# Performance work log

Hardware: AMD Instinct MI355X
Metric: run time of the kernel (lower is better)

## Reference

```python
import jax, jax.numpy as jnp
import numpy as np
from jax import lax

N, C, H, W = 4, 256, 64, 64
R = 2          # upsample ratio (scale_factor)
K = 5          # CARAFE up_kernel
COMP = 64      # CARAFEPack compressed_channels
EPS = 1e-5     # BatchNorm eps


def setup_inputs() -> dict:
    key = jax.random.key(0)
    ks = jax.random.split(key, 8)
    w = lambda k, s: jax.random.normal(k, s, jnp.float32) * 0.05
    return {
        "low_feature": jax.random.normal(ks[0], (N, C, H * R, W * R), jnp.float32),
        "high_feature": jax.random.normal(ks[1], (N, C, H, W), jnp.float32),
        "w_cc": w(ks[2], (COMP, C, 1, 1)),            # channel compressor 1x1
        "b_cc": jnp.zeros((COMP,), jnp.float32),
        "w_ce": w(ks[3], (K * K * R * R, COMP, 3, 3)), # content encoder 3x3
        "b_ce": jnp.zeros((K * K * R * R,), jnp.float32),
        "w_conv2": w(ks[4], (C, C, 1, 1)),
        "b_conv2": jnp.zeros((C,), jnp.float32),
        "w_bott": w(ks[5], (C, 2 * C, 1, 1)),          # bottleneck 1x1, no bias
        "gamma": jnp.ones((C,), jnp.float32),
        "beta": jnp.zeros((C,), jnp.float32),
    }


def _conv1x1(x, w, b=None):
    y = jnp.einsum('nchw,oc->nohw', x, w[:, :, 0, 0])
    if b is not None:
        y = y + b[None, :, None, None]
    return y


def _conv3x3(x, w, b):
    y = lax.conv_general_dilated(x, w, (1, 1), [(1, 1), (1, 1)],
                                 dimension_numbers=('NCHW', 'OIHW', 'NCHW'))
    return y + b[None, :, None, None]


def _pixel_shuffle(x, r):
    n, c, h, w = x.shape
    c2 = c // (r * r)
    x = x.reshape(n, c2, r, r, h, w).transpose(0, 1, 4, 2, 5, 3)
    return x.reshape(n, c2, h * r, w * r)


def _carafe(x, w_cc, b_cc, w_ce, b_ce):
    n, c, h, w = x.shape
    # predicted kernels: compress -> encode -> pixel_shuffle -> softmax over k^2
    mask = _conv3x3(_conv1x1(x, w_cc, b_cc), w_ce, b_ce)      # [N, K*K*R*R, H, W]
    mask = _pixel_shuffle(mask, R)                            # [N, K*K, H*R, W*R]
    mask = jax.nn.softmax(mask, axis=1)                       # group=1 -> over K*K
    # k x k neighborhoods of x (zero-padded), kernel index = ky*K + kx
    pad = K // 2
    xp = jnp.pad(x, ((0, 0), (0, 0), (pad, pad), (pad, pad)))
    patches = jnp.stack([xp[:, :, dy:dy + h, dx:dx + w]
                         for dy in range(K) for dx in range(K)], axis=2)  # [N,C,K*K,H,W]
    # each output pixel (i,j) reads source (i//R, j//R) neighborhood
    mr = mask.reshape(n, K * K, h, R, w, R)
    out = jnp.einsum('nckhw,nkhawb->nchawb', patches, mr)
    return out.reshape(n, c, h * R, w * R)


def reference(low_feature, high_feature, w_cc, b_cc, w_ce, b_ce,
              w_conv2, b_conv2, w_bott, gamma, beta):
    hf = _carafe(high_feature, w_cc, b_cc, w_ce, b_ce)        # [N,C,H*R,W*R]
    value = _conv1x1(hf, w_conv2, b_conv2)
    x = jnp.concatenate([value, hf], axis=1)                  # [N,2C,.,.]
    x = _conv1x1(x, w_bott)
    # BatchNorm (training-mode batch statistics) + ReLU
    mean = jnp.mean(x, axis=(0, 2, 3), keepdims=True)
    var = jnp.var(x, axis=(0, 2, 3), keepdims=True)
    x = (x - mean) * lax.rsqrt(var + EPS)
    x = x * gamma[None, :, None, None] + beta[None, :, None, None]
    return jax.nn.relu(x)
```

## Files before the change

### kernel.cpp

```cpp
#include <hip/hip_runtime.h>
#include <hip/hip_bf16.h>

#define N_    4
#define C_    256
#define PS_   4096
#define PO_   16384
#define COMP_ 64
#define QCH_  100

typedef unsigned short u16;
typedef __attribute__((ext_vector_type(8))) short short8;
typedef __attribute__((ext_vector_type(4))) float f32x4;

__device__ __forceinline__ u16 f2bu(float f) {
    __hip_bfloat16 h = __float2bfloat16(f);
    return __builtin_bit_cast(u16, h);
}
__device__ __forceinline__ float bits2f(unsigned u) {
    union { unsigned i; float f; } v; v.i = u; return v.f;
}

__global__ __launch_bounds__(256) void k_prep(const float* __restrict__ w_bott,
        const float* __restrict__ w_conv2, const float* __restrict__ b_conv2,
        const float* __restrict__ w_ce, const float* __restrict__ w_cc,
        u16* __restrict__ Weff_bf, float* __restrict__ beff,
        u16* __restrict__ Wb, u16* __restrict__ Wcc_bf) {
    int bid = blockIdx.x;
    if (bid < 256) {
        int o = bid, c = threadIdx.x;
        __shared__ float wb[512];
        wb[c]       = w_bott[o * 512 + c];
        wb[c + 256] = w_bott[o * 512 + 256 + c];
        __syncthreads();
        float acc = wb[256 + c];
        #pragma unroll 8
        for (int m = 0; m < 256; ++m)
            acc += wb[m] * w_conv2[m * 256 + c];
        Weff_bf[o * 256 + c] = f2bu(acc);
        if (c == 0) {
            float be = 0.f;
            for (int m = 0; m < 256; ++m) be += wb[m] * b_conv2[m];
            beff[o] = be;
        }
    } else if (bid < 544) {
        int i = (bid - 256) * 256 + threadIdx.x;
        int q = i / 576, u = i - q * 576;
        float v = (q < 100) ? w_ce[q * 576 + u] : 0.f;
        Wb[i] = f2bu(v);
    } else {
        int j = (bid - 544) * 256 + threadIdx.x;
        Wcc_bf[j] = f2bu(w_cc[j]);
    }
}

__global__ __launch_bounds__(256) void k_compress_mfma(const u16* __restrict__ Wcc_bf,
        const float* __restrict__ high, const float* __restrict__ b_cc,
        float* __restrict__ comp) {
    int tid = threadIdx.x;
    int wid = tid >> 6, lane = tid & 63;
    int col = lane & 15, quad = lane >> 4;
    int px0 = blockIdx.x * 64;
    int n = px0 >> 12, pxb = px0 & 4095;
    __shared__ u16 As[64 * 40];
    __shared__ u16 Bs[64 * 40];
    f32x4 acc[4] = {};
    #pragma unroll 1
    for (int k0 = 0; k0 < 256; k0 += 32) {
        __syncthreads();
        {
            int row = tid >> 2, seg = tid & 3;
            short8 av = *reinterpret_cast<const short8*>(Wcc_bf + row * 256 + k0 + seg * 8);
            *reinterpret_cast<short8*>(&As[row * 40 + seg * 8]) = av;
        }
        #pragma unroll
        for (int it = 0; it < 4; ++it) {
            int idx = it * 256 + tid;
            int c = (idx >> 6) * 2, px = idx & 63;
            const float* hp = high + (n * C_ + k0 + c) * PS_ + pxb + px;
            unsigned lo = f2bu(hp[0]);
            unsigned hi = f2bu(hp[PS_]);
            *reinterpret_cast<unsigned*>(&Bs[px * 40 + c]) = lo | (hi << 16);
        }
        __syncthreads();
        short8 a = *reinterpret_cast<const short8*>(&As[(wid * 16 + col) * 40 + quad * 8]);
        #pragma unroll
        for (int nt = 0; nt < 4; ++nt) {
            short8 b = *reinterpret_cast<const short8*>(&Bs[(nt * 16 + col) * 40 + quad * 8]);
            acc[nt] = __builtin_amdgcn_mfma_f32_16x16x32_bf16(a, b, acc[nt], 0, 0, 0);
        }
    }
    #pragma unroll
    for (int r = 0; r < 4; ++r) {
        int m = wid * 16 + quad * 4 + r;
        float bias = b_cc[m];
        float* cp = comp + (n * COMP_ + m) * PS_ + pxb + col;
        #pragma unroll
        for (int nt = 0; nt < 4; ++nt)
            cp[nt * 16] = acc[nt][r] + bias;
    }
}

__global__ __launch_bounds__(256) void k_im2col(const float* __restrict__ comp,
        u16* __restrict__ Icol) {
    int b = blockIdx.x;
    int n = b >> 6, tile = b & 63;
    int ty0 = (tile >> 3) << 3, tx0 = (tile & 7) << 3;
    int tid = threadIdx.x;
    __shared__ float ct[64 * 100];
    for (int idx = tid; idx < 6400; idx += 256) {
        int cc = idx / 100, r = idx - cc * 100;
        int yy = ty0 - 1 + r / 10, xx = tx0 - 1 + (r % 10);
        float v = 0.f;
        if ((unsigned)yy < 64u && (unsigned)xx < 64u)
            v = comp[(n * COMP_ + cc) * PS_ + yy * 64 + xx];
        ct[idx] = v;
    }
    __syncthreads();
    int u0 = tid * 2, u1 = u0 + 1;
    int c0 = (unsigned)u0 / 9u, t0 = u0 - c0 * 9;
    int c1 = (unsigned)u1 / 9u, t1 = u1 - c1 * 9;
    int off0 = c0 * 100 + (t0 / 3) * 10 + (t0 % 3);
    int off1 = c1 * 100 + (t1 / 3) * 10 + (t1 % 3);
    int u2 = 512 + tid * 2, u3 = u2 + 1;
    int c2 = (unsigned)u2 / 9u, t2 = u2 - c2 * 9;
    int c3 = (unsigned)u3 / 9u, t3 = u3 - c3 * 9;
    int off2 = c2 * 100 + (t2 / 3) * 10 + (t2 % 3);
    int off3 = c3 * 100 + (t3 / 3) * 10 + (t3 % 3);
    #pragma unroll 1
    for (int px = 0; px < 64; ++px) {
        int py = px >> 3, pxx = px & 7;
        int base = py * 10 + pxx;
        int gpx = n * PS_ + (ty0 + py) * 64 + tx0 + pxx;
        u16* dst = Icol + gpx * 576;
        unsigned lo = f2bu(ct[off0 + base]);
        unsigned hi = f2bu(ct[off1 + base]);
        *reinterpret_cast<unsigned*>(dst + u0) = lo | (hi << 16);
        if (tid < 32) {
            unsigned lo2 = f2bu(ct[off2 + base]);
            unsigned hi2 = f2bu(ct[off3 + base]);
            *reinterpret_cast<unsigned*>(dst + u2) = lo2 | (hi2 << 16);
        }
    }
}

__global__ __launch_bounds__(256) void k_encode_mfma(const u16* __restrict__ Wb,
        const u16* __restrict__ Icol, const float* __restrict__ b_ce,
        float* __restrict__ mask_raw) {
    int tid = threadIdx.x;
    int wid = tid >> 6, lane = tid & 63;
    int col = lane & 15, quad = lane >> 4;
    int px0 = blockIdx.x * 64;
    int n = px0 >> 12, pxb = px0 & 4095;
    __shared__ u16 As[128 * 40];
    __shared__ u16 Bs[64 * 40];
    f32x4 acc[2][4] = {};
    #pragma unroll 1
    for (int k0 = 0; k0 < 576; k0 += 32) {
        __syncthreads();
        #pragma unroll
        for (int it = 0; it < 2; ++it) {
            int s = tid + it * 256;
            int row = s >> 2, seg = s & 3;
            short8 av = *reinterpret_cast<const short8*>(Wb + row * 576 + k0 + seg * 8);
            *reinterpret_cast<short8*>(&As[row * 40 + seg * 8]) = av;
        }
        {
            int row = tid >> 2, seg = tid & 3;
            short8 bv = *reinterpret_cast<const short8*>(Icol + (px0 + row) * 576 + k0 + seg * 8);
            *reinterpret_cast<short8*>(&Bs[row * 40 + seg * 8]) = bv;
        }
        __syncthreads();
        short8 a0 = *reinterpret_cast<const short8*>(&As[(wid * 32 + col) * 40 + quad * 8]);
        short8 a1 = *reinterpret_cast<const short8*>(&As[(wid * 32 + 16 + col) * 40 + quad * 8]);
        #pragma unroll
        for (int nt = 0; nt < 4; ++nt) {
            short8 b = *reinterpret_cast<const short8*>(&Bs[(nt * 16 + col) * 40 + quad * 8]);
            acc[0][nt] = __builtin_amdgcn_mfma_f32_16x16x32_bf16(a0, b, acc[0][nt], 0, 0, 0);
            acc[1][nt] = __builtin_amdgcn_mfma_f32_16x16x32_bf16(a1, b, acc[1][nt], 0, 0, 0);
        }
    }
    #pragma unroll
    for (int mi = 0; mi < 2; ++mi) {
        int qbase = (wid * 2 + mi) * 16 + quad * 4;
        #pragma unroll
        for (int r = 0; r < 4; ++r) {
            int q = qbase + r;
            if (q < 100) {
                float bias = b_ce[q];
                float* mp = mask_raw + (n * QCH_ + q) * PS_ + pxb + col;
                #pragma unroll
                for (int nt = 0; nt < 4; ++nt)
                    mp[nt * 16] = acc[mi][nt][r] + bias;
            }
        }
    }
}

__global__ __launch_bounds__(256) void k_ygemm_mfma(const u16* __restrict__ Weff_bf,
        const float* __restrict__ high, u16* __restrict__ Yt) {
    int tid = threadIdx.x;
    int wid = tid >> 6, lane = tid & 63;
    int col = lane & 15, quad = lane >> 4;
    int px0 = blockIdx.x * 128;
    int o0 = blockIdx.y * 128;
    int n = px0 >> 12, pxb = px0 & 4095;
    __shared__ u16 As[128 * 40];
    __shared__ u16 Bs[128 * 40];
    f32x4 acc[2][8] = {};
    #pragma unroll 1
    for (int k0 = 0; k0 < 256; k0 += 32) {
        __syncthreads();
        #pragma unroll
        for (int it = 0; it < 2; ++it) {
            int s = tid + it * 256;
            int row = s >> 2, seg = s & 3;
            short8 av = *reinterpret_cast<const short8*>(Weff_bf + (o0 + row) * 256 + k0 + seg * 8);
            *reinterpret_cast<short8*>(&As[row * 40 + seg * 8]) = av;
        }
        #pragma unroll
        for (int it = 0; it < 8; ++it) {
            int idx = it * 256 + tid;
            int c = (idx >> 7) * 2, px = idx & 127;
            const float* hp = high + (n * C_ + k0 + c) * PS_ + pxb + px;
            unsigned lo = f2bu(hp[0]);
            unsigned hi = f2bu(hp[PS_]);
            *reinterpret_cast<unsigned*>(&Bs[px * 40 + c]) = lo | (hi << 16);
        }
        __syncthreads();
        short8 a0 = *reinterpret_cast<const short8*>(&As[(wid * 32 + col) * 40 + quad * 8]);
        short8 a1 = *reinterpret_cast<const short8*>(&As[(wid * 32 + 16 + col) * 40 + quad * 8]);
        #pragma unroll
        for (int nt = 0; nt < 8; ++nt) {
            short8 b = *reinterpret_cast<const short8*>(&Bs[(nt * 16 + col) * 40 + quad * 8]);
            acc[0][nt] = __builtin_amdgcn_mfma_f32_16x16x32_bf16(a0, b, acc[0][nt], 0, 0, 0);
            acc[1][nt] = __builtin_amdgcn_mfma_f32_16x16x32_bf16(a1, b, acc[1][nt], 0, 0, 0);
        }
    }
    #pragma unroll
    for (int mi = 0; mi < 2; ++mi) {
        int ob = o0 + wid * 32 + mi * 16 + quad * 4;
        #pragma unroll
        for (int nt = 0; nt < 8; ++nt) {
            int gpx = px0 + nt * 16 + col;
            unsigned lo = f2bu(acc[mi][nt][0]) | ((unsigned)f2bu(acc[mi][nt][1]) << 16);
            unsigned hi = f2bu(acc[mi][nt][2]) | ((unsigned)f2bu(acc[mi][nt][3]) << 16);
            uint2 pk; pk.x = lo; pk.y = hi;
            *reinterpret_cast<uint2*>(Yt + (size_t)gpx * 256 + ob) = pk;
        }
    }
}

__global__ __launch_bounds__(256, 4) void k_carafe(const u16* __restrict__ Yt,
        const float* __restrict__ mask_raw, const float* __restrict__ beff,
        float* __restrict__ xout, float* __restrict__ ps, float* __restrict__ pq) {
    int tile = blockIdx.x, n = blockIdx.y, zq = blockIdx.z;
    int sh0 = (tile >> 3) << 3, sw0 = (tile & 7) << 3;
    int tid = threadIdx.x;
    int px = tid & 63, g = tid >> 6;
    int ly = px >> 3, lx = px & 7;
    int h = sh0 + ly, w = sw0 + lx;
    int sp = (g & 1) << 1;
    int cg = (g >> 1) << 5;
    int ch0 = zq << 6;

    __shared__ u16 xt[144 * 68];

    const u16* Yb = Yt + (size_t)n * PS_ * 256;
    for (int idx = tid; idx < 1152; idx += 256) {
        int spix = idx >> 3, seg = idx & 7;
        int row = spix / 12, colm = spix - row * 12;
        int yy = sh0 - 2 + row, xx = sw0 - 2 + colm;
        short8 val = {};
        if ((unsigned)yy < 64u && (unsigned)xx < 64u)
            val = *reinterpret_cast<const short8*>(Yb + (size_t)(yy * 64 + xx) * 256 + ch0 + seg * 8);
        *reinterpret_cast<short8*>(&xt[spix * 68 + seg * 8]) = val;
    }

    float vs[2][25];
    {
        const float* mb = mask_raw + ((size_t)n * QCH_ + sp) * PS_ + h * 64 + w;
        #pragma unroll
        for (int j = 0; j < 2; ++j) {
            #pragma unroll
            for (int k = 0; k < 25; ++k)
                vs[j][k] = mb[(size_t)(k * 4 + j) * PS_];
            float mx = vs[j][0];
            #pragma unroll
            for (int k = 1; k < 25; ++k) mx = fmaxf(mx, vs[j][k]);
            float sum = 0.f;
            #pragma unroll
            for (int k = 0; k < 25; ++k) { vs[j][k] = __expf(vs[j][k] - mx); sum += vs[j][k]; }
            float inv = 1.f / sum;
            #pragma unroll
            for (int k = 0; k < 25; ++k) vs[j][k] *= inv;
        }
    }
    __syncthreads();

    const u16* bp = xt + (ly * 12 + lx) * 68;
    int row_off = (2 * h + (sp >> 1)) * 128 + 2 * w;
    int slot = (n * 64 + tile) * 2 + (g & 1);
    float* hp_base = xout + (size_t)n * C_ * PO_;

    #pragma unroll 1
    for (int cq = 0; cq < 8; ++cq) {
        int c = cg + cq * 4;
        int ch = ch0 + c;
        f32x4 bv = *reinterpret_cast<const f32x4*>(beff + ch);
        float a0[4] = {bv[0], bv[1], bv[2], bv[3]};
        float a1[4] = {bv[0], bv[1], bv[2], bv[3]};
        const u16* tp = bp + c;
        #pragma unroll
        for (int ky = 0; ky < 5; ++ky) {
            #pragma unroll
            for (int kx = 0; kx < 5; ++kx) {
                uint2 rv = *reinterpret_cast<const uint2*>(tp + (ky * 12 + kx) * 68);
                float f0 = bits2f(rv.x << 16);
                float f1 = bits2f(rv.x & 0xffff0000u);
                float f2 = bits2f(rv.y << 16);
                float f3 = bits2f(rv.y & 0xffff0000u);
                int k = ky * 5 + kx;
                float m0 = vs[0][k], m1 = vs[1][k];
                a0[0] += m0 * f0; a0[1] += m0 * f1;
                a0[2] += m0 * f2; a0[3] += m0 * f3;
                a1[0] += m1 * f0; a1[1] += m1 * f1;
                a1[2] += m1 * f2; a1[3] += m1 * f3;
            }
        }
        #pragma unroll
        for (int i = 0; i < 4; ++i) {
            float2 r; r.x = a0[i]; r.y = a1[i];
            *reinterpret_cast<float2*>(hp_base + (size_t)(ch + i) * PO_ + row_off) = r;
        }
        #pragma unroll
        for (int i = 0; i < 4; ++i) {
            float s  = a0[i] + a1[i];
            float q2 = a0[i] * a0[i] + a1[i] * a1[i];
            #pragma unroll
            for (int off = 1; off < 64; off <<= 1) {
                s  += __shfl_xor(s, off);
                q2 += __shfl_xor(q2, off);
            }
            if (px == 0) {
                ps[(ch + i) * 512 + slot] = s;
                pq[(ch + i) * 512 + slot] = q2;
            }
        }
    }
}

__global__ __launch_bounds__(256) void k_stats(const float* __restrict__ ps,
        const float* __restrict__ pq, const float* __restrict__ gamma,
        const float* __restrict__ beta, float* __restrict__ scale,
        float* __restrict__ shift) {
    int o = blockIdx.x, tid = threadIdx.x;
    float s = ps[o * 512 + tid] + ps[o * 512 + 256 + tid];
    float q = pq[o * 512 + tid] + pq[o * 512 + 256 + tid];
    __shared__ float rs[256], rq[256];
    rs[tid] = s; rq[tid] = q;
    __syncthreads();
    for (int off = 128; off > 0; off >>= 1) {
        if (tid < off) { rs[tid] += rs[tid + off]; rq[tid] += rq[tid + off]; }
        __syncthreads();
    }
    if (tid == 0) {
        float mean = rs[0] * (1.f / 65536.f);
        float var  = rq[0] * (1.f / 65536.f) - mean * mean;
        float sc = rsqrtf(var + 1e-5f) * gamma[o];
        scale[o] = sc;
        shift[o] = beta[o] - mean * sc;
    }
}

__global__ __launch_bounds__(256) void k_norm(float* __restrict__ xb,
        const float* __restrict__ scale, const float* __restrict__ shift) {
    int base = (blockIdx.x * 256 + threadIdx.x) * 4;
    int o = (base >> 14) & 255;
    float sc = scale[o], sh = shift[o];
    float4 v = *reinterpret_cast<const float4*>(xb + base);
    v.x = fmaxf(v.x * sc + sh, 0.f);
    v.y = fmaxf(v.y * sc + sh, 0.f);
    v.z = fmaxf(v.z * sc + sh, 0.f);
    v.w = fmaxf(v.w * sc + sh, 0.f);
    *reinterpret_cast<float4*>(xb + base) = v;
}

extern "C" void kernel_launch(void* const* d_in, const int* in_sizes, int n_in,
                              void* d_out, int out_size, void* d_ws, size_t ws_size,
                              hipStream_t stream) {
    const float* high    = (const float*)d_in[1];
    const float* w_cc    = (const float*)d_in[2];
    const float* b_cc    = (const float*)d_in[3];
    const float* w_ce    = (const float*)d_in[4];
    const float* b_ce    = (const float*)d_in[5];
    const float* w_conv2 = (const float*)d_in[6];
    const float* b_conv2 = (const float*)d_in[7];
    const float* w_bott  = (const float*)d_in[8];
    const float* gamma   = (const float*)d_in[9];
    const float* beta    = (const float*)d_in[10];

    char* ws = (char*)d_ws;
    float* beff    = (float*)(ws + 0);
    float* scale   = (float*)(ws + 1024);
    float* shift   = (float*)(ws + 2048);
    u16*   Weff_bf = (u16*)  (ws + 3072);
    u16*   Wcc_bf  = (u16*)  (ws + 134144);
    u16*   Wb      = (u16*)  (ws + 166912);
    float* mask    = (float*)(ws + 314368);
    float* comp    = (float*)(ws + 314368);
    u16*   Icol    = (u16*)  (ws + 6867968);
    u16*   Yt      = (u16*)  (ws + 6867968);
    float* ps      = (float*)(ws + 15256576);
    float* pq      = (float*)(ws + 15780864);
    float* xout    = (float*)d_out;

    k_prep         <<<608, 256, 0, stream>>>(w_bott, w_conv2, b_conv2, w_ce, w_cc,
                                             Weff_bf, beff, Wb, Wcc_bf);
    k_compress_mfma<<<256, 256, 0, stream>>>(Wcc_bf, high, b_cc, comp);
    k_im2col       <<<256, 256, 0, stream>>>(comp, Icol);
    k_encode_mfma  <<<256, 256, 0, stream>>>(Wb, Icol, b_ce, mask);
    k_ygemm_mfma   <<<dim3(128, 2), 256, 0, stream>>>(Weff_bf, high, Yt);
    k_carafe       <<<dim3(64, 4, 4), 256, 0, stream>>>(Yt, mask, beff, xout, ps, pq);
    k_stats        <<<256, 256, 0, stream>>>(ps, pq, gamma, beta, scale, shift);
    k_norm         <<<16384, 256, 0, stream>>>(xout, scale, shift);
}
```

Measured before the change: 294.9 us.

## Retile CARAFE blocks, stage mask in LDS, and fuse BN stats with normalize

The CARAFE kernel now uses 4x8 source tiles with 8 warps covering two upsample rows and 128 channels in two 64-channel chunks. Mask logits are staged once into shared memory so the softmax reads come from LDS instead of strided global loads. Partial statistics are written as per-slot channel vectors, and the stats reduction is fused with the normalize+ReLU pass into a single kernel, removing one launch and the scale/shift round trip. The smaller tiles raise halo overhead (96 halo pixels for 32 outputs), and each k_bn block reduces the stats redundantly once per batch.

```diff
diff --git a/kernel.cpp b/kernel.cpp
--- a/kernel.cpp
+++ b/kernel.cpp
@@ -253,109 +253,120 @@
 __global__ __launch_bounds__(256, 4) void k_carafe(const u16* __restrict__ Yt,
         const float* __restrict__ mask_raw, const float* __restrict__ beff,
         float* __restrict__ xout, float* __restrict__ ps, float* __restrict__ pq) {
-    int tile = blockIdx.x, n = blockIdx.y, zq = blockIdx.z;
-    int sh0 = (tile >> 3) << 3, sw0 = (tile & 7) << 3;
-    int tid = threadIdx.x;
-    int px = tid & 63, g = tid >> 6;
+    int tile = blockIdx.x, n = blockIdx.y, zh = blockIdx.z;
+    int sh0 = (tile >> 3) * 4, sw0 = (tile & 7) * 8;
+    int tid = threadIdx.x;
+    int px = tid & 31, g = tid >> 5;
     int ly = px >> 3, lx = px & 7;
     int h = sh0 + ly, w = sw0 + lx;
-    int sp = (g & 1) << 1;
-    int cg = (g >> 1) << 5;
-    int ch0 = zq << 6;
-
-    __shared__ u16 xt[144 * 68];
+    int spp = g & 1;
+    int sp = spp * 2;
+    int cg = g >> 1;
+
+    __shared__ float mt[100 * 32];
+    __shared__ u16 xt[96 * 68];
+
+    for (int idx = tid; idx < 3200; idx += 256) {
+        int q = idx >> 5, p = idx & 31;
+        mt[idx] = mask_raw[(n * QCH_ + q) * PS_ + (sh0 + (p >> 3)) * 64 + sw0 + (p & 7)];
+    }
+    __syncthreads();
+
+    float vs[2][25];
+    #pragma unroll
+    for (int j = 0; j < 2; ++j) {
+        float mx = -1e30f;
+        #pragma unroll
+        for (int k = 0; k < 25; ++k) {
+            vs[j][k] = mt[(k * 4 + sp + j) * 32 + px];
+            mx = fmaxf(mx, vs[j][k]);
+        }
+        float sum = 0.f;
+        #pragma unroll
+        for (int k = 0; k < 25; ++k) { vs[j][k] = __expf(vs[j][k] - mx); sum += vs[j][k]; }
+        float inv = 1.f / sum;
+        #pragma unroll
+        for (int k = 0; k < 25; ++k) vs[j][k] *= inv;
+    }
 
     const u16* Yb = Yt + (size_t)n * PS_ * 256;
-    for (int idx = tid; idx < 1152; idx += 256) {
-        int spix = idx >> 3, seg = idx & 7;
-        int row = spix / 12, colm = spix - row * 12;
-        int yy = sh0 - 2 + row, xx = sw0 - 2 + colm;
-        short8 val = {};
-        if ((unsigned)yy < 64u && (unsigned)xx < 64u)
-            val = *reinterpret_cast<const short8*>(Yb + (size_t)(yy * 64 + xx) * 256 + ch0 + seg * 8);
-        *reinterpret_cast<short8*>(&xt[spix * 68 + seg * 8]) = val;
-    }
-
-    float vs[2][25];
-    {
-        const float* mb = mask_raw + ((size_t)n * QCH_ + sp) * PS_ + h * 64 + w;
-        #pragma unroll
-        for (int j = 0; j < 2; ++j) {
+    int ch_base = zh * 128;
+    int row_off = (2 * h + spp) * 128 + 2 * w;
+    int slot = n * 128 + tile;
+    float* hp_base = xout + (size_t)n * C_ * PO_;
+
+    #pragma unroll 1
+    for (int chunk = 0; chunk < 2; ++chunk) {
+        int ch0 = ch_base + chunk * 64;
+        __syncthreads();
+        for (int idx = tid; idx < 768; idx += 256) {
+            int spix = idx >> 3, seg = idx & 7;
+            int row = spix / 12, colm = spix - row * 12;
+            int yy = sh0 - 2 + row, xx = sw0 - 2 + colm;
+            short8 val = {};
+            if ((unsigned)yy < 64u && (unsigned)xx < 64u)
+                val = *reinterpret_cast<const short8*>(Yb + (size_t)(yy * 64 + xx) * 256 + ch0 + seg * 8);
+            *reinterpret_cast<short8*>(&xt[spix * 68 + seg * 8]) = val;
+        }
+        __syncthreads();
+
+        #pragma unroll 1
+        for (int cq = 0; cq < 4; ++cq) {
+            int c = cg * 16 + cq * 4;
+            int ch = ch0 + c;
+            f32x4 bv = *reinterpret_cast<const f32x4*>(beff + ch);
+            float a0[4] = {bv[0], bv[1], bv[2], bv[3]};
+            float a1[4] = {bv[0], bv[1], bv[2], bv[3]};
+            const u16* tp = xt + (ly * 12 + lx) * 68 + c;
             #pragma unroll
-            for (int k = 0; k < 25; ++k)
-                vs[j][k] = mb[(size_t)(k * 4 + j) * PS_];
-            float mx = vs[j][0];
+            for (int ky = 0; ky < 5; ++ky) {
+                #pragma unroll
+                for (int kx = 0; kx < 5; ++kx) {
+                    uint2 rv = *reinterpret_cast<const uint2*>(tp + (ky * 12 + kx) * 68);
+                    float f0 = bits2f(rv.x << 16);
+                    float f1 = bits2f(rv.x & 0xffff0000u);
+                    float f2 = bits2f(rv.y << 16);
+                    float f3 = bits2f(rv.y & 0xffff0000u);
+                    int k = ky * 5 + kx;
+                    float m0 = vs[0][k], m1 = vs[1][k];
+                    a0[0] += m0 * f0; a0[1] += m0 * f1;
+                    a0[2] += m0 * f2; a0[3] += m0 * f3;
+                    a1[0] += m1 * f0; a1[1] += m1 * f1;
+                    a1[2] += m1 * f2; a1[3] += m1 * f3;
+                }
+            }
             #pragma unroll
-            for (int k = 1; k < 25; ++k) mx = fmaxf(mx, vs[j][k]);
-            float sum = 0.f;
+            for (int i = 0; i < 4; ++i) {
+                float2 r; r.x = a0[i]; r.y = a1[i];
+                *reinterpret_cast<float2*>(hp_base + (size_t)(ch + i) * PO_ + row_off) = r;
+            }
+            f32x4 sv, qv;
             #pragma unroll
-            for (int k = 0; k < 25; ++k) { vs[j][k] = __expf(vs[j][k] - mx); sum += vs[j][k]; }
-            float inv = 1.f / sum;
-            #pragma unroll
-            for (int k = 0; k < 25; ++k) vs[j][k] *= inv;
-        }
-    }
-    __syncthreads();
-
-    const u16* bp = xt + (ly * 12 + lx) * 68;
-    int row_off = (2 * h + (sp >> 1)) * 128 + 2 * w;
-    int slot = (n * 64 + tile) * 2 + (g & 1);
-    float* hp_base = xout + (size_t)n * C_ * PO_;
-
-    #pragma unroll 1
-    for (int cq = 0; cq < 8; ++cq) {
-        int c = cg + cq * 4;
-        int ch = ch0 + c;
-        f32x4 bv = *reinterpret_cast<const f32x4*>(beff + ch);
-        float a0[4] = {bv[0], bv[1], bv[2], bv[3]};
-        float a1[4] = {bv[0], bv[1], bv[2], bv[3]};
-        const u16* tp = bp + c;
-        #pragma unroll
-        for (int ky = 0; ky < 5; ++ky) {
-            #pragma unroll
-            for (int kx = 0; kx < 5; ++kx) {
-                uint2 rv = *reinterpret_cast<const uint2*>(tp + (ky * 12 + kx) * 68);
-                float f0 = bits2f(rv.x << 16);
-                float f1 = bits2f(rv.x & 0xffff0000u);
-                float f2 = bits2f(rv.y << 16);
-                float f3 = bits2f(rv.y & 0xffff0000u);
-                int k = ky * 5 + kx;
-                float m0 = vs[0][k], m1 = vs[1][k];
-                a0[0] += m0 * f0; a0[1] += m0 * f1;
-                a0[2] += m0 * f2; a0[3] += m0 * f3;
-                a1[0] += m1 * f0; a1[1] += m1 * f1;
-                a1[2] += m1 * f2; a1[3] += m1 * f3;
+            for (int i = 0; i < 4; ++i) {
+                float s  = a0[i] + a1[i];
+                float q2 = a0[i] * a0[i] + a1[i] * a1[i];
+                #pragma unroll
+                for (int off = 1; off < 64; off <<= 1) {
+                    s  += __shfl_xor(s, off);
+                    q2 += __shfl_xor(q2, off);
+                }
+                sv[i] = s; qv[i] = q2;
             }
-        }
-        #pragma unroll
-        for (int i = 0; i < 4; ++i) {
-            float2 r; r.x = a0[i]; r.y = a1[i];
-            *reinterpret_cast<float2*>(hp_base + (size_t)(ch + i) * PO_ + row_off) = r;
-        }
-        #pragma unroll
-        for (int i = 0; i < 4; ++i) {
-            float s  = a0[i] + a1[i];
-            float q2 = a0[i] * a0[i] + a1[i] * a1[i];
-            #pragma unroll
-            for (int off = 1; off < 64; off <<= 1) {
-                s  += __shfl_xor(s, off);
-                q2 += __shfl_xor(q2, off);
+            if ((tid & 63) == 0) {
+                *reinterpret_cast<f32x4*>(ps + slot * 256 + ch) = sv;
+                *reinterpret_cast<f32x4*>(pq + slot * 256 + ch) = qv;
             }
-            if (px == 0) {
-                ps[(ch + i) * 512 + slot] = s;
-                pq[(ch + i) * 512 + slot] = q2;
-            }
-        }
-    }
-}
-
-__global__ __launch_bounds__(256) void k_stats(const float* __restrict__ ps,
+        }
+    }
+}
+
+__global__ __launch_bounds__(256) void k_bn(const float* __restrict__ ps,
         const float* __restrict__ pq, const float* __restrict__ gamma,
-        const float* __restrict__ beta, float* __restrict__ scale,
-        float* __restrict__ shift) {
-    int o = blockIdx.x, tid = threadIdx.x;
-    float s = ps[o * 512 + tid] + ps[o * 512 + 256 + tid];
-    float q = pq[o * 512 + tid] + pq[o * 512 + 256 + tid];
+        const float* __restrict__ beta, float* __restrict__ xb) {
+    int o = blockIdx.x >> 2, n = blockIdx.x & 3;
+    int tid = threadIdx.x;
+    float s = ps[tid * 256 + o] + ps[(tid + 256) * 256 + o];
+    float q = pq[tid * 256 + o] + pq[(tid + 256) * 256 + o];
     __shared__ float rs[256], rq[256];
     rs[tid] = s; rq[tid] = q;
     __syncthreads();
@@ -363,26 +374,26 @@
         if (tid < off) { rs[tid] += rs[tid + off]; rq[tid] += rq[tid + off]; }
         __syncthreads();
     }
+    __shared__ float sc_s, sh_s;
     if (tid == 0) {
         float mean = rs[0] * (1.f / 65536.f);
         float var  = rq[0] * (1.f / 65536.f) - mean * mean;
         float sc = rsqrtf(var + 1e-5f) * gamma[o];
-        scale[o] = sc;
-        shift[o] = beta[o] - mean * sc;
-    }
-}
-
-__global__ __launch_bounds__(256) void k_norm(float* __restrict__ xb,
-        const float* __restrict__ scale, const float* __restrict__ shift) {
-    int base = (blockIdx.x * 256 + threadIdx.x) * 4;
-    int o = (base >> 14) & 255;
-    float sc = scale[o], sh = shift[o];
-    float4 v = *reinterpret_cast<const float4*>(xb + base);
-    v.x = fmaxf(v.x * sc + sh, 0.f);
-    v.y = fmaxf(v.y * sc + sh, 0.f);
-    v.z = fmaxf(v.z * sc + sh, 0.f);
-    v.w = fmaxf(v.w * sc + sh, 0.f);
-    *reinterpret_cast<float4*>(xb + base) = v;
+        sc_s = sc;
+        sh_s = beta[o] - mean * sc;
+    }
+    __syncthreads();
+    float sc = sc_s, sh = sh_s;
+    float* p = xb + (size_t)(n * C_ + o) * PO_;
+    #pragma unroll 4
+    for (int i = tid * 4; i < PO_; i += 1024) {
+        float4 v = *reinterpret_cast<const float4*>(p + i);
+        v.x = fmaxf(v.x * sc + sh, 0.f);
+        v.y = fmaxf(v.y * sc + sh, 0.f);
+        v.z = fmaxf(v.z * sc + sh, 0.f);
+        v.w = fmaxf(v.w * sc + sh, 0.f);
+        *reinterpret_cast<float4*>(p + i) = v;
+    }
 }
 
 extern "C" void kernel_launch(void* const* d_in, const int* in_sizes, int n_in,
@@ -401,8 +412,6 @@
 
     char* ws = (char*)d_ws;
     float* beff    = (float*)(ws + 0);
-    float* scale   = (float*)(ws + 1024);
-    float* shift   = (float*)(ws + 2048);
     u16*   Weff_bf = (u16*)  (ws + 3072);
     u16*   Wcc_bf  = (u16*)  (ws + 134144);
     u16*   Wb      = (u16*)  (ws + 166912);
@@ -420,7 +429,6 @@
     k_im2col       <<<256, 256, 0, stream>>>(comp, Icol);
     k_encode_mfma  <<<256, 256, 0, stream>>>(Wb, Icol, b_ce, mask);
     k_ygemm_mfma   <<<dim3(128, 2), 256, 0, stream>>>(Weff_bf, high, Yt);
-    k_carafe       <<<dim3(64, 4, 4), 256, 0, stream>>>(Yt, mask, beff, xout, ps, pq);
-    k_stats        <<<256, 256, 0, stream>>>(ps, pq, gamma, beta, scale, shift);
-    k_norm         <<<16384, 256, 0, stream>>>(xout, scale, shift);
-}
+    k_carafe       <<<dim3(128, 4, 2), 256, 0, stream>>>(Yt, mask, beff, xout, ps, pq);
+    k_bn           <<<1024, 256, 0, stream>>>(ps, pq, gamma, beta, xout);
+}
```

After: 324.3 us. +10.0%, slower.
